# Kernel tuning notes

Measured on AMD Instinct MI355X. Metric: run time of the kernel, lower is better.

The kernel has to match this reference:

```python
import jax, jax.numpy as jnp
import numpy as np

H = 8  # num_heads (init kwarg)

def setup_inputs() -> dict:
    key = jax.random.key(0)
    k1, k2, k3 = jax.random.split(key, 3)
    B, N, C = 1, 256, 512
    x = jax.random.normal(k1, (B, N, C), dtype=jnp.float32)
    W_att = jax.random.normal(k2, (C, 5 * C), dtype=jnp.float32) * 0.02
    b_att = jnp.zeros((5 * C,), dtype=jnp.float32)
    W_out = jax.random.normal(k3, (C, C), dtype=jnp.float32) * 0.02
    b_out = jnp.zeros((C,), dtype=jnp.float32)
    return {"x": x, "W_att": W_att, "b_att": b_att, "W_out": W_out, "b_out": b_out}

def reference(x, W_att, b_att, W_out, b_out):
    B, N, C = x.shape
    D = C // H
    scale = D ** -0.5
    # att_proj: [B,N,5C] -> rearrange 'b n (h d)' with h=H -> [B,H,N,5D] -> chunk 5
    p = (x @ W_att + b_att).reshape(B, N, H, 5 * D).transpose(0, 2, 1, 3)
    q, kj, kk, vj, vk = jnp.split(p, 5, axis=-1)  # each [B,H,N,D]
    # third-order scores: [B,H,N,N,N]
    scores = jnp.einsum('bhid,bhjd,bhkd->bhijk', q, kj, kk) * scale
    # softmax over flattened (j,k) per query i
    w = jax.nn.softmax(scores.reshape(B, H, N, N * N), axis=-1).reshape(B, H, N, N, N)
    y = jnp.einsum('bhijk,bhjd,bhkd->bhid', w, vj, vk)  # [B,H,N,D]
    y = y.transpose(0, 2, 1, 3).reshape(B, N, C)  # 'b h n d -> b n (h d)'
    return y @ W_out + b_out
```

## Files before the change

kernel.cpp:

```cpp
#include <hip/hip_runtime.h>
#include <stdint.h>


typedef __attribute__((ext_vector_type(4))) float f32x4;
typedef __attribute__((ext_vector_type(4))) short s16x4;
typedef __attribute__((ext_vector_type(8))) short s16x8;

#define H_ 8
#define N_ 256
#define D_ 64
#define C_ 512
#define NC5 2560
#define SCALE_LOG2E 0.1803368801111204f

__device__ __forceinline__ unsigned short f2bf_rne(float x) {
  union { float f; unsigned u; } a; a.f = x;
  unsigned r = a.u + 0x7fffu + ((a.u >> 16) & 1u);
  return (unsigned short)(r >> 16);
}

__device__ __forceinline__ unsigned pk_bf16(float a, float b) {
#if __has_builtin(__builtin_amdgcn_cvt_pk_bf16_f32)
  typedef __attribute__((ext_vector_type(2))) __bf16 bf16x2;
  union { bf16x2 v; unsigned u; } u;
  u.v = __builtin_amdgcn_cvt_pk_bf16_f32(a, b);
  return u.u;
#else
  return (unsigned)f2bf_rne(a) | ((unsigned)f2bf_rne(b) << 16);
#endif
}

__device__ __forceinline__ f32x4 mfma32(s16x8 a, s16x8 b, f32x4 c) {
  return __builtin_amdgcn_mfma_f32_16x16x32_bf16(a, b, c, 0, 0, 0);
}

__device__ __forceinline__ f32x4 mfma16(s16x4 a, s16x4 b, f32x4 c) {
#if __has_builtin(__builtin_amdgcn_mfma_f32_16x16x16bf16_1k)
  return __builtin_amdgcn_mfma_f32_16x16x16bf16_1k(a, b, c, 0, 0, 0);
#else
  asm volatile("s_nop 1\n\t"
               "v_mfma_f32_16x16x16_bf16 %0, %1, %2, %0\n\t"
               "s_nop 7\n\t"
               "s_nop 2"
               : "+v"(c) : "v"(a), "v"(b));
  return c;
#endif
}

__global__ __launch_bounds__(256) void proj_kernel(
    const float* __restrict__ x, const float* __restrict__ W,
    const float* __restrict__ b,
    float* __restrict__ qS, float* __restrict__ kj,
    unsigned short* __restrict__ kkB, float* __restrict__ vj,
    float* __restrict__ vkT) {
  __shared__ float As[32][17];
  __shared__ float Bs[32][68];
  const int bx = blockIdx.x;
  const int by = blockIdx.y;
  const int tid = threadIdx.x;
  const int m = tid >> 4;
  const int c4 = (tid & 15) * 4;
  float acc0 = 0.f, acc1 = 0.f, acc2 = 0.f, acc3 = 0.f;

  const int lk = tid & 31;
  const int lm = tid >> 5;
  const int bk = tid >> 4;

  for (int k0 = 0; k0 < C_; k0 += 32) {
    As[lk][lm] = x[(by * 16 + lm) * C_ + k0 + lk];
    As[lk][lm + 8] = x[(by * 16 + lm + 8) * C_ + k0 + lk];
    *(f32x4*)&Bs[bk][c4] = *(const f32x4*)&W[(k0 + bk) * NC5 + bx * 64 + c4];
    *(f32x4*)&Bs[bk + 16][c4] =
        *(const f32x4*)&W[(k0 + bk + 16) * NC5 + bx * 64 + c4];
    __syncthreads();
#pragma unroll
    for (int kq = 0; kq < 32; ++kq) {
      float a = As[kq][m];
      f32x4 bv = *(const f32x4*)&Bs[kq][c4];
      acc0 += a * bv.x; acc1 += a * bv.y; acc2 += a * bv.z; acc3 += a * bv.w;
    }
    __syncthreads();
  }

  const int i = by * 16 + m;
  const int col0 = bx * 64 + c4;
  const int h = (bx * 64) / 320;
  const int part = ((bx * 64) % 320) >> 6;
  const int d0 = c4;
  float v0 = acc0 + b[col0 + 0];
  float v1 = acc1 + b[col0 + 1];
  float v2 = acc2 + b[col0 + 2];
  float v3 = acc3 + b[col0 + 3];
  const int idx = (h * N_ + i) * D_ + d0;
  if (part == 0) {
    f32x4 o = {v0 * SCALE_LOG2E, v1 * SCALE_LOG2E, v2 * SCALE_LOG2E,
               v3 * SCALE_LOG2E};
    *(f32x4*)(qS + idx) = o;
  } else if (part == 1) {
    f32x4 o = {v0, v1, v2, v3};
    *(f32x4*)(kj + idx) = o;
  } else if (part == 2) {
    union { unsigned u[2]; s16x4 v4; } t;
    t.u[0] = pk_bf16(v0, v1);
    t.u[1] = pk_bf16(v2, v3);
    *(s16x4*)(kkB + idx) = t.v4;
  } else if (part == 3) {
    f32x4 o = {v0, v1, v2, v3};
    *(f32x4*)(vj + idx) = o;
  } else {
    vkT[(h * D_ + d0 + 0) * N_ + i] = v0;
    vkT[(h * D_ + d0 + 1) * N_ + i] = v1;
    vkT[(h * D_ + d0 + 2) * N_ + i] = v2;
    vkT[(h * D_ + d0 + 3) * N_ + i] = v3;
  }
}

__global__ __launch_bounds__(256, 2) void flash3_kernel(
    const float* __restrict__ qS,
    const float* __restrict__ kjF,
    const unsigned short* __restrict__ kkB,
    const float* __restrict__ vjF,
    const float* __restrict__ vkT,
    float* __restrict__ slab,
    float* __restrict__ lslab) {
  const int h = blockIdx.z;
  const int ic = blockIdx.y;
  const int jc = blockIdx.x;
  const int wave = threadIdx.x >> 6;
  const int lane = threadIdx.x & 63;
  const int q = lane >> 4;
  const int c = lane & 15;
  const int i0 = ic * 64;

  const float* qh = qS + h * (N_ * D_);
  const float* kjh = kjF + h * (N_ * D_);
  const unsigned short* kkh = kkB + h * (N_ * D_);
  const float* vjh = vjF + h * (N_ * D_);
  const float* vkh = vkT + h * (D_ * N_);

  f32x4 acc[4][4];
#pragma unroll
  for (int mb = 0; mb < 4; ++mb)
#pragma unroll
    for (int nb = 0; nb < 4; ++nb) acc[mb][nb] = (f32x4){0.f, 0.f, 0.f, 0.f};
  float lac[4] = {0.f, 0.f, 0.f, 0.f};

  for (int jj = 0; jj < 2; ++jj) {
    const int j = jc * 8 + wave * 2 + jj;
    const f32x4 kj0a = *(const f32x4*)(kjh + j * D_ + q * 8);
    const f32x4 kj0b = *(const f32x4*)(kjh + j * D_ + q * 8 + 4);
    const f32x4 kj1a = *(const f32x4*)(kjh + j * D_ + 32 + q * 8);
    const f32x4 kj1b = *(const f32x4*)(kjh + j * D_ + 32 + q * 8 + 4);
    float vjv[4];
#pragma unroll
    for (int mb = 0; mb < 4; ++mb) vjv[mb] = vjh[j * D_ + mb * 16 + c];

    s16x8 qf[4][2];
#pragma unroll
    for (int nb = 0; nb < 4; ++nb) {
      const float* qp = qh + (i0 + nb * 16 + c) * D_;
      f32x4 a0 = *(const f32x4*)(qp + q * 8);
      f32x4 a1 = *(const f32x4*)(qp + q * 8 + 4);
      f32x4 b0 = *(const f32x4*)(qp + 32 + q * 8);
      f32x4 b1 = *(const f32x4*)(qp + 32 + q * 8 + 4);
      union { unsigned u[4]; s16x8 v; } t0, t1;
      t0.u[0] = pk_bf16(a0.x * kj0a.x, a0.y * kj0a.y);
      t0.u[1] = pk_bf16(a0.z * kj0a.z, a0.w * kj0a.w);
      t0.u[2] = pk_bf16(a1.x * kj0b.x, a1.y * kj0b.y);
      t0.u[3] = pk_bf16(a1.z * kj0b.z, a1.w * kj0b.w);
      t1.u[0] = pk_bf16(b0.x * kj1a.x, b0.y * kj1a.y);
      t1.u[1] = pk_bf16(b0.z * kj1a.z, b0.w * kj1a.w);
      t1.u[2] = pk_bf16(b1.x * kj1b.x, b1.y * kj1b.y);
      t1.u[3] = pk_bf16(b1.z * kj1b.z, b1.w * kj1b.w);
      qf[nb][0] = t0.v;
      qf[nb][1] = t1.v;
    }

    for (int k0 = 0; k0 < N_; k0 += 64) {
#pragma unroll
      for (int mb = 0; mb < 4; ++mb) {
        const unsigned short* kp = kkh + (k0 + mb * 16 + c) * D_;
        s16x8 ka0 = *(const s16x8*)(kp + q * 8);
        s16x8 ka1 = *(const s16x8*)(kp + 32 + q * 8);
        f32x4 fv[4];
#pragma unroll
        for (int md = 0; md < 4; ++md)
          fv[md] =
              *(const f32x4*)(vkh + (md * 16 + c) * N_ + k0 + mb * 16 + q * 4);

        f32x4 st[4];
#pragma unroll
        for (int nb = 0; nb < 4; ++nb) {
          f32x4 z = (f32x4){0.f, 0.f, 0.f, 0.f};
          z = mfma32(ka0, qf[nb][0], z);
          z = mfma32(ka1, qf[nb][1], z);
          st[nb] = z;
        }
        s16x4 pn[4];
#pragma unroll
        for (int nb = 0; nb < 4; ++nb) {
          float p0 = __builtin_exp2f(st[nb].x);
          float p1 = __builtin_exp2f(st[nb].y);
          float p2 = __builtin_exp2f(st[nb].z);
          float p3 = __builtin_exp2f(st[nb].w);
          lac[nb] += (p0 + p1) + (p2 + p3);
          union { unsigned u[2]; s16x4 v4; } t;
          t.u[0] = pk_bf16(p0, p1);
          t.u[1] = pk_bf16(p2, p3);
          pn[nb] = t.v4;
        }
#pragma unroll
        for (int md = 0; md < 4; ++md) {
          float s = vjv[md];
          union { unsigned u[2]; s16x4 v4; } t;
          t.u[0] = pk_bf16(fv[md].x * s, fv[md].y * s);
          t.u[1] = pk_bf16(fv[md].z * s, fv[md].w * s);
#pragma unroll
          for (int nb = 0; nb < 4; ++nb)
            acc[md][nb] = mfma16(t.v4, pn[nb], acc[md][nb]);
        }
      }
    }
  }

  __shared__ float red[2][64 * 68];
  __shared__ float lredA[2][64];
  __shared__ float lredB[64];

  float lv[4];
#pragma unroll
  for (int nb = 0; nb < 4; ++nb) {
    float v = lac[nb];
    v += __shfl_xor(v, 16);
    v += __shfl_xor(v, 32);
    lv[nb] = v;
  }

  if (wave >= 2) {
    float* dst = red[wave - 2];
#pragma unroll
    for (int mb = 0; mb < 4; ++mb)
#pragma unroll
      for (int nb = 0; nb < 4; ++nb)
        *(f32x4*)&dst[(nb * 16 + c) * 68 + mb * 16 + q * 4] = acc[mb][nb];
    if (q == 0)
#pragma unroll
      for (int nb = 0; nb < 4; ++nb) lredA[wave - 2][nb * 16 + c] = lv[nb];
  }
  __syncthreads();
  if (wave < 2) {
    const float* src = red[wave];
#pragma unroll
    for (int mb = 0; mb < 4; ++mb)
#pragma unroll
      for (int nb = 0; nb < 4; ++nb)
        acc[mb][nb] += *(const f32x4*)&src[(nb * 16 + c) * 68 + mb * 16 + q * 4];
    if (q == 0)
#pragma unroll
      for (int nb = 0; nb < 4; ++nb) lv[nb] += lredA[wave][nb * 16 + c];
  }
  __syncthreads();
  if (wave == 1) {
#pragma unroll
    for (int mb = 0; mb < 4; ++mb)
#pragma unroll
      for (int nb = 0; nb < 4; ++nb)
        *(f32x4*)&red[0][(nb * 16 + c) * 68 + mb * 16 + q * 4] = acc[mb][nb];
    if (q == 0)
#pragma unroll
      for (int nb = 0; nb < 4; ++nb) lredB[nb * 16 + c] = lv[nb];
  }
  __syncthreads();
  if (wave == 0) {
    float* out = slab + ((h * 32 + jc) * 4 + ic) * 4096;
#pragma unroll
    for (int mb = 0; mb < 4; ++mb)
#pragma unroll
      for (int nb = 0; nb < 4; ++nb) {
        f32x4 v = acc[mb][nb] +
                  *(const f32x4*)&red[0][(nb * 16 + c) * 68 + mb * 16 + q * 4];
        *(f32x4*)(out + (nb * 16 + c) * 64 + mb * 16 + q * 4) = v;
      }
    if (q == 0)
#pragma unroll
      for (int nb = 0; nb < 4; ++nb)
        lslab[(h * 32 + jc) * 256 + ic * 64 + nb * 16 + c] =
            lv[nb] + lredB[nb * 16 + c];
  }
}

__global__ __launch_bounds__(256) void reduce_kernel(
    const float* __restrict__ slab, const float* __restrict__ lslab,
    float* __restrict__ yn) {
  int idx = blockIdx.x * 256 + threadIdx.x;
  int h = idx >> 12;
  int r = idx & 4095;
  int ic = r >> 10;
  int il = (r >> 4) & 63;
  int d4 = (r & 15) * 4;
  f32x4 s = {0.f, 0.f, 0.f, 0.f};
  float l = 0.f;
#pragma unroll 4
  for (int jc = 0; jc < 32; ++jc) {
    s += *(const f32x4*)&slab[(((h * 32 + jc) * 4 + ic) << 12) + il * 64 + d4];
    l += lslab[(h * 32 + jc) * 256 + ic * 64 + il];
  }
  int i = ic * 64 + il;
  float rl = 1.f / l;
  f32x4 o = {s.x * rl, s.y * rl, s.z * rl, s.w * rl};
  *(f32x4*)&yn[i * C_ + h * 64 + d4] = o;
}

__global__ __launch_bounds__(256) void out_gemm(
    const float* __restrict__ A, const float* __restrict__ W,
    const float* __restrict__ b, float* __restrict__ out) {
  __shared__ float As[32][17];
  __shared__ float Bs[32][68];
  const int bx = blockIdx.x;
  const int by = blockIdx.y;
  const int tid = threadIdx.x;
  const int m = tid >> 4;
  const int c4 = (tid & 15) * 4;
  float acc0 = 0.f, acc1 = 0.f, acc2 = 0.f, acc3 = 0.f;

  const int lk = tid & 31;
  const int lm = tid >> 5;
  const int bk = tid >> 4;

  for (int k0 = 0; k0 < C_; k0 += 32) {
    As[lk][lm] = A[(by * 16 + lm) * C_ + k0 + lk];
    As[lk][lm + 8] = A[(by * 16 + lm + 8) * C_ + k0 + lk];
    *(f32x4*)&Bs[bk][c4] = *(const f32x4*)&W[(k0 + bk) * C_ + bx * 64 + c4];
    *(f32x4*)&Bs[bk + 16][c4] =
        *(const f32x4*)&W[(k0 + bk + 16) * C_ + bx * 64 + c4];
    __syncthreads();
#pragma unroll
    for (int kq = 0; kq < 32; ++kq) {
      float a = As[kq][m];
      f32x4 bv = *(const f32x4*)&Bs[kq][c4];
      acc0 += a * bv.x; acc1 += a * bv.y; acc2 += a * bv.z; acc3 += a * bv.w;
    }
    __syncthreads();
  }

  const int i = by * 16 + m;
  const int col = bx * 64 + c4;
  f32x4 o = {acc0 + b[col + 0], acc1 + b[col + 1], acc2 + b[col + 2],
             acc3 + b[col + 3]};
  *(f32x4*)(out + i * C_ + col) = o;
}

extern "C" void kernel_launch(void* const* d_in, const int* in_sizes, int n_in,
                              void* d_out, int out_size, void* d_ws,
                              size_t ws_size, hipStream_t stream) {
  const float* x     = (const float*)d_in[0];
  const float* W_att = (const float*)d_in[1];
  const float* b_att = (const float*)d_in[2];
  const float* W_out = (const float*)d_in[3];
  const float* b_out = (const float*)d_in[4];

  char* ws = (char*)d_ws;
  float* slab           = (float*)(ws + 0);
  float* lslab          = (float*)(ws + 16777216);
  float* qSb            = (float*)(ws + 17039360);
  float* kj             = (float*)(ws + 17563648);
  unsigned short* kkB   = (unsigned short*)(ws + 18087936);
  float* vj             = (float*)(ws + 18350080);
  float* vkT            = (float*)(ws + 18874368);
  float* yn             = (float*)(ws + 19398656);

  proj_kernel<<<dim3(40, 16), 256, 0, stream>>>(x, W_att, b_att, qSb, kj, kkB,
                                                vj, vkT);
  flash3_kernel<<<dim3(32, 4, 8), 256, 0, stream>>>(qSb, kj, kkB, vj, vkT,
                                                    slab, lslab);
  reduce_kernel<<<dim3(128), 256, 0, stream>>>(slab, lslab, yn);
  out_gemm<<<dim3(8, 16), 256, 0, stream>>>(yn, W_out, b_out, (float*)d_out);
}
```

Baseline: 222.5 us.

## Factor vj scaling out of inner loop using split per-j accumulators and bf16 vk

Stores vk as pre-converted bf16 so the inner loop loads half the bytes and skips the per-element multiply-and-pack. The vj scale, constant for each j, is factored out of the inner loop: each wave keeps separate accumulators for its two j values and applies the vj scales once after the loop. This doubles the accumulator registers (32 f32x4 instead of 16), which risks spilling or lower occupancy under the launch bounds of 2 blocks per SM. The rounding also changes, since vk is rounded to bf16 before the vj scale is applied rather than after.

```diff
diff --git a/kernel.cpp b/kernel.cpp
--- a/kernel.cpp
+++ b/kernel.cpp
@@ -52,7 +52,7 @@
     const float* __restrict__ b,
     float* __restrict__ qS, float* __restrict__ kj,
     unsigned short* __restrict__ kkB, float* __restrict__ vj,
-    float* __restrict__ vkT) {
+    unsigned short* __restrict__ vkBT) {
   __shared__ float As[32][17];
   __shared__ float Bs[32][68];
   const int bx = blockIdx.x;
@@ -108,10 +108,10 @@
     f32x4 o = {v0, v1, v2, v3};
     *(f32x4*)(vj + idx) = o;
   } else {
-    vkT[(h * D_ + d0 + 0) * N_ + i] = v0;
-    vkT[(h * D_ + d0 + 1) * N_ + i] = v1;
-    vkT[(h * D_ + d0 + 2) * N_ + i] = v2;
-    vkT[(h * D_ + d0 + 3) * N_ + i] = v3;
+    vkBT[(h * D_ + d0 + 0) * N_ + i] = f2bf_rne(v0);
+    vkBT[(h * D_ + d0 + 1) * N_ + i] = f2bf_rne(v1);
+    vkBT[(h * D_ + d0 + 2) * N_ + i] = f2bf_rne(v2);
+    vkBT[(h * D_ + d0 + 3) * N_ + i] = f2bf_rne(v3);
   }
 }
 
@@ -120,12 +120,12 @@
     const float* __restrict__ kjF,
     const unsigned short* __restrict__ kkB,
     const float* __restrict__ vjF,
-    const float* __restrict__ vkT,
+    const unsigned short* __restrict__ vkBT,
     float* __restrict__ slab,
     float* __restrict__ lslab) {
+  const int jc = blockIdx.x;
+  const int ic = blockIdx.y;
   const int h = blockIdx.z;
-  const int ic = blockIdx.y;
-  const int jc = blockIdx.x;
   const int wave = threadIdx.x >> 6;
   const int lane = threadIdx.x & 63;
   const int q = lane >> 4;
@@ -136,13 +136,17 @@
   const float* kjh = kjF + h * (N_ * D_);
   const unsigned short* kkh = kkB + h * (N_ * D_);
   const float* vjh = vjF + h * (N_ * D_);
-  const float* vkh = vkT + h * (D_ * N_);
-
-  f32x4 acc[4][4];
-#pragma unroll
-  for (int mb = 0; mb < 4; ++mb)
-#pragma unroll
-    for (int nb = 0; nb < 4; ++nb) acc[mb][nb] = (f32x4){0.f, 0.f, 0.f, 0.f};
+  const unsigned short* vkh = vkBT + h * (D_ * N_);
+
+  f32x4 accA[4][4];
+  f32x4 accB[4][4];
+#pragma unroll
+  for (int md = 0; md < 4; ++md)
+#pragma unroll
+    for (int nb = 0; nb < 4; ++nb) {
+      accA[md][nb] = (f32x4){0.f, 0.f, 0.f, 0.f};
+      accB[md][nb] = (f32x4){0.f, 0.f, 0.f, 0.f};
+    }
   float lac[4] = {0.f, 0.f, 0.f, 0.f};
 
   for (int jj = 0; jj < 2; ++jj) {
@@ -151,9 +155,6 @@
     const f32x4 kj0b = *(const f32x4*)(kjh + j * D_ + q * 8 + 4);
     const f32x4 kj1a = *(const f32x4*)(kjh + j * D_ + 32 + q * 8);
     const f32x4 kj1b = *(const f32x4*)(kjh + j * D_ + 32 + q * 8 + 4);
-    float vjv[4];
-#pragma unroll
-    for (int mb = 0; mb < 4; ++mb) vjv[mb] = vjh[j * D_ + mb * 16 + c];
 
     s16x8 qf[4][2];
 #pragma unroll
@@ -182,11 +183,11 @@
         const unsigned short* kp = kkh + (k0 + mb * 16 + c) * D_;
         s16x8 ka0 = *(const s16x8*)(kp + q * 8);
         s16x8 ka1 = *(const s16x8*)(kp + 32 + q * 8);
-        f32x4 fv[4];
+        s16x4 av[4];
 #pragma unroll
         for (int md = 0; md < 4; ++md)
-          fv[md] =
-              *(const f32x4*)(vkh + (md * 16 + c) * N_ + k0 + mb * 16 + q * 4);
+          av[md] =
+              *(const s16x4*)(vkh + (md * 16 + c) * N_ + k0 + mb * 16 + q * 4);
 
         f32x4 st[4];
 #pragma unroll
@@ -209,18 +210,32 @@
           t.u[1] = pk_bf16(p2, p3);
           pn[nb] = t.v4;
         }
-#pragma unroll
-        for (int md = 0; md < 4; ++md) {
-          float s = vjv[md];
-          union { unsigned u[2]; s16x4 v4; } t;
-          t.u[0] = pk_bf16(fv[md].x * s, fv[md].y * s);
-          t.u[1] = pk_bf16(fv[md].z * s, fv[md].w * s);
-#pragma unroll
-          for (int nb = 0; nb < 4; ++nb)
-            acc[md][nb] = mfma16(t.v4, pn[nb], acc[md][nb]);
+        if (jj == 0) {
+#pragma unroll
+          for (int md = 0; md < 4; ++md)
+#pragma unroll
+            for (int nb = 0; nb < 4; ++nb)
+              accA[md][nb] = mfma16(av[md], pn[nb], accA[md][nb]);
+        } else {
+#pragma unroll
+          for (int md = 0; md < 4; ++md)
+#pragma unroll
+            for (int nb = 0; nb < 4; ++nb)
+              accB[md][nb] = mfma16(av[md], pn[nb], accB[md][nb]);
         }
       }
     }
+  }
+
+  const int j0 = jc * 8 + wave * 2;
+  f32x4 yv[4][4];
+#pragma unroll
+  for (int md = 0; md < 4; ++md) {
+    const f32x4 vs0 = *(const f32x4*)(vjh + j0 * D_ + md * 16 + q * 4);
+    const f32x4 vs1 = *(const f32x4*)(vjh + (j0 + 1) * D_ + md * 16 + q * 4);
+#pragma unroll
+    for (int nb = 0; nb < 4; ++nb)
+      yv[md][nb] = accA[md][nb] * vs0 + accB[md][nb] * vs1;
   }
 
   __shared__ float red[2][64 * 68];
@@ -242,7 +257,7 @@
     for (int mb = 0; mb < 4; ++mb)
 #pragma unroll
       for (int nb = 0; nb < 4; ++nb)
-        *(f32x4*)&dst[(nb * 16 + c) * 68 + mb * 16 + q * 4] = acc[mb][nb];
+        *(f32x4*)&dst[(nb * 16 + c) * 68 + mb * 16 + q * 4] = yv[mb][nb];
     if (q == 0)
 #pragma unroll
       for (int nb = 0; nb < 4; ++nb) lredA[wave - 2][nb * 16 + c] = lv[nb];
@@ -254,7 +269,7 @@
     for (int mb = 0; mb < 4; ++mb)
 #pragma unroll
       for (int nb = 0; nb < 4; ++nb)
-        acc[mb][nb] += *(const f32x4*)&src[(nb * 16 + c) * 68 + mb * 16 + q * 4];
+        yv[mb][nb] += *(const f32x4*)&src[(nb * 16 + c) * 68 + mb * 16 + q * 4];
     if (q == 0)
 #pragma unroll
       for (int nb = 0; nb < 4; ++nb) lv[nb] += lredA[wave][nb * 16 + c];
@@ -265,7 +280,7 @@
     for (int mb = 0; mb < 4; ++mb)
 #pragma unroll
       for (int nb = 0; nb < 4; ++nb)
-        *(f32x4*)&red[0][(nb * 16 + c) * 68 + mb * 16 + q * 4] = acc[mb][nb];
+        *(f32x4*)&red[0][(nb * 16 + c) * 68 + mb * 16 + q * 4] = yv[mb][nb];
     if (q == 0)
 #pragma unroll
       for (int nb = 0; nb < 4; ++nb) lredB[nb * 16 + c] = lv[nb];
@@ -277,7 +292,7 @@
     for (int mb = 0; mb < 4; ++mb)
 #pragma unroll
       for (int nb = 0; nb < 4; ++nb) {
-        f32x4 v = acc[mb][nb] +
+        f32x4 v = yv[mb][nb] +
                   *(const f32x4*)&red[0][(nb * 16 + c) * 68 + mb * 16 + q * 4];
         *(f32x4*)(out + (nb * 16 + c) * 64 + mb * 16 + q * 4) = v;
       }
@@ -366,12 +381,12 @@
   float* kj             = (float*)(ws + 17563648);
   unsigned short* kkB   = (unsigned short*)(ws + 18087936);
   float* vj             = (float*)(ws + 18350080);
-  float* vkT            = (float*)(ws + 18874368);
+  unsigned short* vkBT  = (unsigned short*)(ws + 18874368);
   float* yn             = (float*)(ws + 19398656);
 
   proj_kernel<<<dim3(40, 16), 256, 0, stream>>>(x, W_att, b_att, qSb, kj, kkB,
-                                                vj, vkT);
-  flash3_kernel<<<dim3(32, 4, 8), 256, 0, stream>>>(qSb, kj, kkB, vj, vkT,
+                                                vj, vkBT);
+  flash3_kernel<<<dim3(32, 4, 8), 256, 0, stream>>>(qSb, kj, kkB, vj, vkBT,
                                                     slab, lslab);
   reduce_kernel<<<dim3(128), 256, 0, stream>>>(slab, lslab, yn);
   out_gemm<<<dim3(8, 16), 256, 0, stream>>>(yn, W_out, b_out, (float*)d_out);
```

After: 464.5 us. 2.09x slower.
